# Optimization experiments

Hardware: AMD Instinct MI355X
Metric: run time of the kernel (lower is better)

The kernel has to match this reference:

```python
import jax, jax.numpy as jnp
import numpy as np

D_MODEL = 1024
NUM_HEADS = 16
HEAD_DIM = D_MODEL // NUM_HEADS
ROPE_BASE = 10000.0


def _rope_cos_sin(seq_len, head_dim, dtype):
    # inv_freq over half the head dim (standard 1D RoPE)
    inv_freq = 1.0 / (ROPE_BASE ** (jnp.arange(0, head_dim, 2, dtype=jnp.float32) / head_dim))
    ang = jnp.arange(seq_len, dtype=jnp.float32)[:, None] * inv_freq[None, :]  # [S, hd/2]
    cos = jnp.concatenate([jnp.cos(ang), jnp.cos(ang)], axis=-1).astype(dtype)  # [S, hd]
    sin = jnp.concatenate([jnp.sin(ang), jnp.sin(ang)], axis=-1).astype(dtype)
    return cos, sin


def _rotate_half(t):
    t1, t2 = jnp.split(t, 2, axis=-1)
    return jnp.concatenate([-t2, t1], axis=-1)


def _apply_rope(t, cos, sin):
    # t: [B, H, S, hd]; cos/sin: [S, hd]
    return t * cos[None, None, :, :] + _rotate_half(t) * sin[None, None, :, :]


def setup_inputs() -> dict:
    key = jax.random.key(0)
    k1, k2, k3 = jax.random.split(key, 3)
    B, S = 2, 2048
    x = jax.random.normal(k1, (B, S, D_MODEL), dtype=jnp.float32)
    w_qkv = jax.random.normal(k2, (D_MODEL, 3 * D_MODEL), dtype=jnp.float32) * (D_MODEL ** -0.5)
    w_proj = jax.random.normal(k3, (D_MODEL, D_MODEL), dtype=jnp.float32) * (D_MODEL ** -0.5)
    b_proj = jnp.zeros((D_MODEL,), dtype=jnp.float32)
    return {"x": x, "w_qkv": w_qkv, "w_proj": w_proj, "b_proj": b_proj, "causal": 1}


def reference(x, w_qkv, w_proj, b_proj, causal):
    B, S, D = x.shape
    scale = HEAD_DIM ** -0.5
    qkv = x @ w_qkv  # [B, S, 3D]
    q, k, v = jnp.split(qkv, 3, axis=-1)

    def to_heads(t):
        return t.reshape(B, S, NUM_HEADS, HEAD_DIM).transpose(0, 2, 1, 3)  # [B,H,S,hd]

    q, k, v = to_heads(q), to_heads(k), to_heads(v)

    cos, sin = _rope_cos_sin(S, HEAD_DIM, x.dtype)
    q = _apply_rope(q, cos, sin)
    k = _apply_rope(k, cos, sin)

    attn = jnp.einsum('bhqd,bhkd->bhqk', q, k) * scale  # [B,H,S,S]
    if causal:
        causal_mask = jnp.triu(jnp.ones((S, S), dtype=bool), k=1)
        attn = jnp.where(causal_mask[None, None, :, :], jnp.float32(-jnp.inf).astype(attn.dtype), attn)
    attn = jax.nn.softmax(attn, axis=-1)
    out = jnp.einsum('bhqk,bhkd->bhqd', attn, v)  # [B,H,S,hd]
    out = out.transpose(0, 2, 1, 3).reshape(B, S, D)
    return out @ w_proj + b_proj
```

## Files before the change

### kernel.cpp

```cpp
#include <hip/hip_runtime.h>
#include <stdint.h>
#include <math.h>

#define B_   2
#define S_   2048
#define D_   1024
#define H_   16
#define HD_  64
#define M_   (B_*S_)
#define N3_  (3*D_)

typedef __bf16 bf16;
typedef __bf16 bf16x2 __attribute__((ext_vector_type(2)));
typedef __bf16 bf16x4v __attribute__((ext_vector_type(4)));
typedef __bf16 bf16x8 __attribute__((ext_vector_type(8)));
typedef float  f32x4 __attribute__((ext_vector_type(4)));
typedef float  f32x16 __attribute__((ext_vector_type(16)));

__device__ __forceinline__ void gload_lds16(const void* g, void* l) {
  __builtin_amdgcn_global_load_lds(
      (__attribute__((address_space(1))) const unsigned int*)g,
      (__attribute__((address_space(3))) unsigned int*)l, 16, 0, 0);
}

__device__ __forceinline__ float fast_exp2(float x) {
  return __builtin_amdgcn_exp2f(x);
}

__global__ __launch_bounds__(256) void prep_kernel(const float* __restrict__ x, bf16* __restrict__ xb,
                                                   const float* __restrict__ w_qkv, bf16* __restrict__ wqkvT,
                                                   const float* __restrict__ w_proj, bf16* __restrict__ wprojT,
                                                   float* __restrict__ cosT, float* __restrict__ sinT) {
  __shared__ float tile[32][33];
  int blk = blockIdx.x, tid = threadIdx.x;
  if (blk < 1024) {
#pragma unroll
    for (int it = 0; it < 4; it++) {
      int i = (blk * 4 + it) * 256 + tid;
      float4 v = ((const float4*)x)[i];
      bf16x4v o;
      o[0] = (bf16)v.x; o[1] = (bf16)v.y; o[2] = (bf16)v.z; o[3] = (bf16)v.w;
      *(bf16x4v*)(xb + (size_t)i * 4) = o;
    }
  } else if (blk < 5120) {
    const float* in; bf16* out; int R, C, tb;
    if (blk < 4096) { in = w_qkv;  out = wqkvT;  R = 1024; C = 3072; tb = blk - 1024; }
    else            { in = w_proj; out = wprojT; R = 1024; C = 1024; tb = blk - 4096; }
    int nbx = C >> 5;
    int bx = tb % nbx, by = tb / nbx;
    int c0 = bx * 32, r0 = by * 32;
    int tx = tid & 31, ty = tid >> 5;
#pragma unroll
    for (int j = 0; j < 4; j++)
      tile[ty + j * 8][tx] = in[(size_t)(r0 + ty + j * 8) * C + c0 + tx];
    __syncthreads();
#pragma unroll
    for (int j = 0; j < 4; j++)
      out[(size_t)(c0 + ty + j * 8) * R + r0 + tx] = (bf16)tile[tx][ty + j * 8];
  } else {
    int i = (blk - 5120) * 256 + tid;
    int s = i >> 5, d = i & 31;
    float inv = powf(10000.0f, -(float)d * (1.0f / 32.0f));
    float a = (float)s * inv;
    float sv, cv;
    sincosf(a, &sv, &cv);
    cosT[i] = cv; sinT[i] = sv;
  }
}

__global__ __launch_bounds__(512, 2) void gemm_qkv(const bf16* __restrict__ A,
                                                   const bf16* __restrict__ Bt,
                                                   bf16* __restrict__ Cb,
                                                   const float* __restrict__ cosT,
                                                   const float* __restrict__ sinT,
                                                   bf16* __restrict__ vt) {
  __shared__ __align__(16) unsigned char lds[131072];
  const int K = 1024;
  int tid = threadIdx.x, lane = tid & 63, w = tid >> 6;
  int wm = w >> 2, wn = w & 3;
  int bid = blockIdx.y * gridDim.x + blockIdx.x;
  int sw = (bid & 7) * 24 + (bid >> 3);
  int bx = sw % 12, by = sw / 12;
  int m0 = by * 256, n0 = bx * 256;
  int rl = lane & 15, kg = lane >> 4;

  int l3 = lane >> 3;
  int cS = ((lane & 7) ^ l3) * 16;
  const char* sA = (const char*)A  + ((size_t)(m0 + w * 32 + l3) * K) * 2 + cS;
  const char* sB = (const char*)Bt + ((size_t)(n0 + w * 32 + l3) * K) * 2 + cS;
  char* dA = (char*)lds + w * 4096 + lane * 16;
  char* dB = dA + 32768;

#define STG(kt, s)                                                                   \
  do {                                                                               \
    const int _j = (s) & 3;                                                          \
    const int _bo = ((kt) & 1) << 16;                                                \
    if ((s) < 4) gload_lds16(sA + (size_t)_j * 16384 + (size_t)(kt) * 128,           \
                             dA + _bo + _j * 1024);                                  \
    else         gload_lds16(sB + (size_t)_j * 16384 + (size_t)(kt) * 128,           \
                             dB + _bo + _j * 1024);                                  \
  } while (0)

  int chunkv[2];
  chunkv[0] = ((0 + kg) ^ (rl & 7)) * 16;
  chunkv[1] = ((4 + kg) ^ (rl & 7)) * 16;
  int base_a = (wm * 128 + rl) * 128;
  int base_b = 32768 + (wn * 64 + rl) * 128;

#define RDA(Lb, ar, ks) (*(const bf16x8*)((Lb) + base_a + (ar) * 2048 + chunkv[ks]))
#define RDB(Lb, br, ks) (*(const bf16x8*)((Lb) + base_b + (br) * 2048 + chunkv[ks]))
#define BARR() asm volatile("s_barrier" ::: "memory")
#define VM2()  asm volatile("s_waitcnt vmcnt(2)" ::: "memory")

  f32x4 acc[8][4] = {};
  bf16x8 a[4][2], b[4][2];

#pragma unroll
  for (int s = 0; s < 8; s++) { STG(0, s); STG(1, s); }
  asm volatile("s_waitcnt vmcnt(0)" ::: "memory");
  BARR();

  for (int i = 0; i < 8; i++) {
    int t0 = 2 * i, t1 = t0 + 1;
    const char* L0 = (const char*)lds;
    const char* L1 = (const char*)lds + 65536;

    VM2();
#pragma unroll
    for (int ar = 0; ar < 4; ar++) { a[ar][0] = RDA(L0, ar, 0); a[ar][1] = RDA(L0, ar, 1); }
#pragma unroll
    for (int br = 0; br < 2; br++) { b[br][0] = RDB(L0, br, 0); b[br][1] = RDB(L0, br, 1); }
    if (i) { STG(t1, 2); STG(t1, 3); }
    BARR();
    __builtin_amdgcn_s_setprio(1);
#pragma unroll
    for (int ar = 0; ar < 4; ar++)
#pragma unroll
      for (int br = 0; br < 2; br++) {
        acc[ar][br] = __builtin_amdgcn_mfma_f32_16x16x32_bf16(a[ar][0], b[br][0], acc[ar][br], 0, 0, 0);
        acc[ar][br] = __builtin_amdgcn_mfma_f32_16x16x32_bf16(a[ar][1], b[br][1], acc[ar][br], 0, 0, 0);
      }
    __builtin_amdgcn_s_setprio(0);
    BARR();

#pragma unroll
    for (int br = 2; br < 4; br++) { b[br][0] = RDB(L0, br, 0); b[br][1] = RDB(L0, br, 1); }
    if (i) { STG(t1, 4); STG(t1, 5); }
    BARR();
    __builtin_amdgcn_s_setprio(1);
#pragma unroll
    for (int ar = 0; ar < 4; ar++)
#pragma unroll
      for (int br = 2; br < 4; br++) {
        acc[ar][br] = __builtin_amdgcn_mfma_f32_16x16x32_bf16(a[ar][0], b[br][0], acc[ar][br], 0, 0, 0);
        acc[ar][br] = __builtin_amdgcn_mfma_f32_16x16x32_bf16(a[ar][1], b[br][1], acc[ar][br], 0, 0, 0);
      }
    __builtin_amdgcn_s_setprio(0);
    BARR();

#pragma unroll
    for (int ar = 0; ar < 4; ar++) { a[ar][0] = RDA(L0, ar + 4, 0); a[ar][1] = RDA(L0, ar + 4, 1); }
    if (i) { STG(t1, 6); STG(t1, 7); }
    BARR();
    __builtin_amdgcn_s_setprio(1);
#pragma unroll
    for (int ar = 0; ar < 4; ar++)
#pragma unroll
      for (int br = 0; br < 2; br++) {
        acc[ar + 4][br] = __builtin_amdgcn_mfma_f32_16x16x32_bf16(a[ar][0], b[br][0], acc[ar + 4][br], 0, 0, 0);
        acc[ar + 4][br] = __builtin_amdgcn_mfma_f32_16x16x32_bf16(a[ar][1], b[br][1], acc[ar + 4][br], 0, 0, 0);
      }
    __builtin_amdgcn_s_setprio(0);
    BARR();

    if (t0 + 2 < 16) { STG(t0 + 2, 0); STG(t0 + 2, 1); }
    BARR();
    __builtin_amdgcn_s_setprio(1);
#pragma unroll
    for (int ar = 0; ar < 4; ar++)
#pragma unroll
      for (int br = 2; br < 4; br++) {
        acc[ar + 4][br] = __builtin_amdgcn_mfma_f32_16x16x32_bf16(a[ar][0], b[br][0], acc[ar + 4][br], 0, 0, 0);
        acc[ar + 4][br] = __builtin_amdgcn_mfma_f32_16x16x32_bf16(a[ar][1], b[br][1], acc[ar + 4][br], 0, 0, 0);
      }
    __builtin_amdgcn_s_setprio(0);
    BARR();

    VM2();
#pragma unroll
    for (int ar = 0; ar < 4; ar++) { a[ar][0] = RDA(L1, ar, 0); a[ar][1] = RDA(L1, ar, 1); }
#pragma unroll
    for (int br = 0; br < 2; br++) { b[br][0] = RDB(L1, br, 0); b[br][1] = RDB(L1, br, 1); }
    if (t0 + 2 < 16) { STG(t0 + 2, 2); STG(t0 + 2, 3); }
    BARR();
    __builtin_amdgcn_s_setprio(1);
#pragma unroll
    for (int ar = 0; ar < 4; ar++)
#pragma unroll
      for (int br = 0; br < 2; br++) {
        acc[ar][br] = __builtin_amdgcn_mfma_f32_16x16x32_bf16(a[ar][0], b[br][0], acc[ar][br], 0, 0, 0);
        acc[ar][br] = __builtin_amdgcn_mfma_f32_16x16x32_bf16(a[ar][1], b[br][1], acc[ar][br], 0, 0, 0);
      }
    __builtin_amdgcn_s_setprio(0);
    BARR();

#pragma unroll
    for (int br = 2; br < 4; br++) { b[br][0] = RDB(L1, br, 0); b[br][1] = RDB(L1, br, 1); }
    if (t0 + 2 < 16) { STG(t0 + 2, 4); STG(t0 + 2, 5); }
    BARR();
    __builtin_amdgcn_s_setprio(1);
#pragma unroll
    for (int ar = 0; ar < 4; ar++)
#pragma unroll
      for (int br = 2; br < 4; br++) {
        acc[ar][br] = __builtin_amdgcn_mfma_f32_16x16x32_bf16(a[ar][0], b[br][0], acc[ar][br], 0, 0, 0);
        acc[ar][br] = __builtin_amdgcn_mfma_f32_16x16x32_bf16(a[ar][1], b[br][1], acc[ar][br], 0, 0, 0);
      }
    __builtin_amdgcn_s_setprio(0);
    BARR();

#pragma unroll
    for (int ar = 0; ar < 4; ar++) { a[ar][0] = RDA(L1, ar + 4, 0); a[ar][1] = RDA(L1, ar + 4, 1); }
    if (t0 + 2 < 16) { STG(t0 + 2, 6); STG(t0 + 2, 7); }
    BARR();
    __builtin_amdgcn_s_setprio(1);
#pragma unroll
    for (int ar = 0; ar < 4; ar++)
#pragma unroll
      for (int br = 0; br < 2; br++) {
        acc[ar + 4][br] = __builtin_amdgcn_mfma_f32_16x16x32_bf16(a[ar][0], b[br][0], acc[ar + 4][br], 0, 0, 0);
        acc[ar + 4][br] = __builtin_amdgcn_mfma_f32_16x16x32_bf16(a[ar][1], b[br][1], acc[ar + 4][br], 0, 0, 0);
      }
    __builtin_amdgcn_s_setprio(0);
    BARR();

    if (t1 + 2 < 16) { STG(t1 + 2, 0); STG(t1 + 2, 1); }
    BARR();
    __builtin_amdgcn_s_setprio(1);
#pragma unroll
    for (int ar = 0; ar < 4; ar++)
#pragma unroll
      for (int br = 2; br < 4; br++) {
        acc[ar + 4][br] = __builtin_amdgcn_mfma_f32_16x16x32_bf16(a[ar][0], b[br][0], acc[ar + 4][br], 0, 0, 0);
        acc[ar + 4][br] = __builtin_amdgcn_mfma_f32_16x16x32_bf16(a[ar][1], b[br][1], acc[ar + 4][br], 0, 0, 0);
      }
    __builtin_amdgcn_s_setprio(0);
    BARR();
  }

  int rq = kg * 4;
  if (n0 < 2048) {
#pragma unroll
    for (int ar = 0; ar < 8; ar++)
#pragma unroll
      for (int r = 0; r < 4; r++) {
        int row = m0 + wm * 128 + ar * 16 + rq + r;
        int srw = row & 2047;
#pragma unroll
        for (int br = 0; br < 2; br++) {
          int d2 = br * 16 + rl;
          float c = cosT[srw * 32 + d2], sn = sinT[srw * 32 + d2];
          float x1 = acc[ar][br][r], x2 = acc[ar][br + 2][r];
          size_t o = (size_t)row * 3072 + n0 + wn * 64 + d2;
          Cb[o]      = (bf16)(x1 * c - x2 * sn);
          Cb[o + 32] = (bf16)(x2 * c + x1 * sn);
        }
      }
  } else {
    int posbase = ((rq & 4) << 1) | ((rq & 8) >> 1);
#pragma unroll
    for (int ar = 0; ar < 8; ar++) {
      int row0 = m0 + wm * 128 + ar * 16;
      int bb = row0 >> 11;
      int sbase = (row0 & 2047) + posbase;
#pragma unroll
      for (int br = 0; br < 4; br++) {
        int col = n0 + wn * 64 + br * 16 + rl - 2048;
        bf16x4v pv;
        pv[0] = (bf16)acc[ar][br][0]; pv[1] = (bf16)acc[ar][br][1];
        pv[2] = (bf16)acc[ar][br][2]; pv[3] = (bf16)acc[ar][br][3];
        *(bf16x4v*)(vt + ((size_t)(bb * 1024 + col)) * 2048 + sbase) = pv;
      }
    }
  }
#undef STG
#undef RDA
#undef RDB
#undef BARR
#undef VM2
}

__global__ __launch_bounds__(256) void gemm_proj(const bf16* __restrict__ A,
                                                 const bf16* __restrict__ Bt,
                                                 float* __restrict__ Cf,
                                                 const float* __restrict__ bias) {
  __shared__ bf16 As[64 * 32];
  __shared__ bf16 Bs[128 * 32];
  const int K = 1024, N = 1024;
  int tid = threadIdx.x;
  int lane = tid & 63, w = tid >> 6;
  int bid = blockIdx.y * gridDim.x + blockIdx.x;
  int sw = (bid & 7) * 64 + (bid >> 3);
  int bx = sw & 7, by = sw >> 3;
  int m0 = by * 64, n0 = bx * 128;
  int m_off = (w >> 1) * 32, n_off = (w & 1) * 64;
  f32x4 acc[2][4] = {};

  const char* Ab = (const char*)A;
  const char* Bb = (const char*)Bt;
  int arow = tid >> 2, achk = (tid & 3) * 16;

  for (int k0 = 0; k0 < K; k0 += 32) {
    gload_lds16(Ab + ((size_t)(m0 + arow) * K + k0) * 2 + achk, (char*)As + tid * 16);
    gload_lds16(Bb + ((size_t)(n0 + arow) * K + k0) * 2 + achk, (char*)Bs + tid * 16);
    gload_lds16(Bb + ((size_t)(n0 + 64 + arow) * K + k0) * 2 + achk, (char*)Bs + 4096 + tid * 16);
    __syncthreads();
    int rl = lane & 15;
    int kgb = (lane >> 4) * 16;
    bf16x8 a[2], b[4];
    for (int i = 0; i < 2; i++)
      a[i] = *(const bf16x8*)((const char*)As + (m_off + i * 16 + rl) * 64 + kgb);
    for (int j = 0; j < 4; j++)
      b[j] = *(const bf16x8*)((const char*)Bs + (n_off + j * 16 + rl) * 64 + kgb);
    for (int i = 0; i < 2; i++)
      for (int j = 0; j < 4; j++)
        acc[i][j] = __builtin_amdgcn_mfma_f32_16x16x32_bf16(a[i], b[j], acc[i][j], 0, 0, 0);
    __syncthreads();
  }

  int rq = (lane >> 4) * 4, cl = lane & 15;
  for (int i = 0; i < 2; i++)
    for (int j = 0; j < 4; j++) {
      int col = n0 + n_off + j * 16 + cl;
      float bv = bias[col];
      for (int r = 0; r < 4; r++) {
        int row = m0 + m_off + i * 16 + rq + r;
        Cf[(size_t)row * N + col] = acc[i][j][r] + bv;
      }
    }
}

__global__ __launch_bounds__(512, 4) void attn_kernel(const bf16* __restrict__ qkv,
                                                      const bf16* __restrict__ vt,
                                                      bf16* __restrict__ O) {
  __shared__ __align__(16) unsigned char Ks[2][16384];
  __shared__ __align__(16) unsigned char Vs[2][16384];
  int tid = threadIdx.x, lane = tid & 63, w = tid >> 6;
  int qw = w & 3, p = w >> 2;
  int bid = blockIdx.x;
  int xcd = bid & 7, slot = bid >> 3;
  int bh = xcd * 4 + (slot & 3);
  int u = slot >> 2;
  int qt = 15 - u;
  int b = bh >> 4, h = bh & 15;
  int q0w = qt * 128 + qw * 32;
  int l31 = lane & 31, hi = lane >> 5;
  const char* qb = (const char*)qkv;
  const char* vb = (const char*)vt;

  int kr0 = tid >> 3, kcs = (tid & 7) ^ (kr0 & 7);
  int vr0 = tid >> 4, vcs = (tid & 15) ^ (vr0 & 7);

#define STAGE(buf, kvbase)                                                                              \
  do {                                                                                                  \
    gload_lds16(qb + (((size_t)(b * 2048 + (kvbase) + kr0) * 3072) + 1024 + h * 64) * 2 + kcs * 16,     \
                (char*)Ks[buf] + tid * 16);                                                             \
    gload_lds16(qb + (((size_t)(b * 2048 + (kvbase) + kr0 + 64) * 3072) + 1024 + h * 64) * 2 + kcs * 16,\
                (char*)Ks[buf] + (tid + 512) * 16);                                                     \
    gload_lds16(vb + (((size_t)(bh * 64 + vr0) * 2048) + (kvbase)) * 2 + vcs * 16,                      \
                (char*)Vs[buf] + tid * 16);                                                             \
    gload_lds16(vb + (((size_t)(bh * 64 + vr0 + 32) * 2048) + (kvbase)) * 2 + vcs * 16,                 \
                (char*)Vs[buf] + (tid + 512) * 16);                                                     \
  } while (0)

  bf16x8 aq[4];
#pragma unroll
  for (int s = 0; s < 4; s++) {
    size_t row = (size_t)(b * 2048 + q0w + l31);
    bf16x8 v = *(const bf16x8*)(qb + (row * 3072 + h * 64 + s * 16 + hi * 8) * 2);
#pragma unroll
    for (int e = 0; e < 8; e++) v[e] = (bf16)((float)v[e] * 0.18033688f);
    aq[s] = v;
  }

  f32x16 o0 = {}, o1 = {};
  float mrun = -3e38f, lrun = 0.f;
  int npair = qt + 1;

  STAGE(0, 0);
  asm volatile("s_waitcnt vmcnt(0)" ::: "memory");
  __builtin_amdgcn_s_barrier();

  for (int i = 0; i < npair; i++) {
    int cur = i & 1;
    if (i + 1 < npair) STAGE(cur ^ 1, (i + 1) * 128);

    int kvw = i * 128 + p * 64;
    if (kvw <= q0w + 31) {
      bool diag = (kvw + 63 > q0w);

      f32x16 scr[2];
#pragma unroll
      for (int kf = 0; kf < 2; kf++)
#pragma unroll
        for (int r = 0; r < 16; r++) scr[kf][r] = 0.f;
      __builtin_amdgcn_s_setprio(1);
#pragma unroll
      for (int s = 0; s < 4; s++) {
#pragma unroll
        for (int kf = 0; kf < 2; kf++) {
          int row = p * 64 + kf * 32 + l31;
          int ch = (hi + 2 * s) ^ (row & 7);
          bf16x8 ak = *(const bf16x8*)(Ks[cur] + row * 128 + ch * 16);
          scr[kf] = __builtin_amdgcn_mfma_f32_32x32x16_bf16(ak, aq[s], scr[kf], 0, 0, 0);
        }
      }
      __builtin_amdgcn_s_setprio(0);

      int qg = q0w + l31;
      if (diag) {
#pragma unroll
        for (int kf = 0; kf < 2; kf++)
#pragma unroll
          for (int r = 0; r < 16; r++) {
            int k = kvw + kf * 32 + (r & 3) + 8 * (r >> 2) + 4 * hi;
            if (k > qg) scr[kf][r] = -3e38f;
          }
      }

      float mx = -3e38f;
#pragma unroll
      for (int kf = 0; kf < 2; kf++)
#pragma unroll
        for (int r = 0; r < 16; r++) mx = fmaxf(mx, scr[kf][r]);
      mx = fmaxf(mx, __shfl_xor(mx, 32));

      if (!__all(mx - mrun <= 11.5f)) {
        float mnew = fmaxf(mrun, mx);
        float corr = exp2f(mrun - mnew);
        mrun = mnew;
        lrun *= corr;
#pragma unroll
        for (int r = 0; r < 16; r++) {
          float cr = __shfl(corr, (r & 3) + 8 * (r >> 2) + 4 * hi);
          o0[r] *= cr; o1[r] *= cr;
        }
      }

      float rs = 0.f;
      unsigned D[2][8];
#pragma unroll
      for (int kf = 0; kf < 2; kf++)
#pragma unroll
        for (int j = 0; j < 8; j++) {
          float p0 = fast_exp2(scr[kf][2 * j] - mrun);
          float p1 = fast_exp2(scr[kf][2 * j + 1] - mrun);
          rs += p0 + p1;
          bf16x2 tp; tp[0] = (bf16)p0; tp[1] = (bf16)p1;
          D[kf][j] = __builtin_bit_cast(unsigned, tp);
        }
      rs += __shfl_xor(rs, 32);
      lrun += rs;

#pragma unroll
      for (int kf = 0; kf < 2; kf++) {
#pragma unroll
        for (int sg = 0; sg < 2; sg++) {
          union { unsigned u4[4]; bf16x8 v; } ap;
          ap.u4[0] = D[kf][4 * sg + 0];
          ap.u4[1] = D[kf][4 * sg + 1];
          ap.u4[2] = D[kf][4 * sg + 2];
          ap.u4[3] = D[kf][4 * sg + 3];
          __builtin_amdgcn_s_setprio(1);
#pragma unroll
          for (int nf = 0; nf < 2; nf++) {
            int row = nf * 32 + l31;
            int ch = ((p * 8) + (hi + 2 * sg + 4 * kf)) ^ (row & 7);
            bf16x8 bv = *(const bf16x8*)(Vs[cur] + row * 256 + ch * 16);
            if (nf == 0) o0 = __builtin_amdgcn_mfma_f32_32x32x16_bf16(ap.v, bv, o0, 0, 0, 0);
            else         o1 = __builtin_amdgcn_mfma_f32_32x32x16_bf16(ap.v, bv, o1, 0, 0, 0);
          }
          __builtin_amdgcn_s_setprio(0);
        }
      }
    }

    asm volatile("s_waitcnt vmcnt(0)" ::: "memory");
    __builtin_amdgcn_s_barrier();
  }

  float* mlb = (float*)Ks;
  if (hi == 0) {
    mlb[((qw * 2 + p) * 2 + 0) * 32 + l31] = mrun;
    mlb[((qw * 2 + p) * 2 + 1) * 32 + l31] = lrun;
  }
  __syncthreads();
  float m_o = mlb[((qw * 2 + (1 - p)) * 2 + 0) * 32 + l31];
  float l_o = mlb[((qw * 2 + (1 - p)) * 2 + 1) * 32 + l31];
  float Mm = fmaxf(mrun, m_o);
  float cs = exp2f(mrun - Mm);
  float L  = lrun * cs + l_o * exp2f(m_o - Mm);
  float* obuf = (float*)Vs;
  if (p == 1) {
#pragma unroll
    for (int r = 0; r < 16; r++) {
      int crow = (r & 3) + 8 * (r >> 2) + 4 * hi;
      float c = __shfl(cs, crow);
      obuf[qw * 2048 + r * 64 + lane]        = o0[r] * c;
      obuf[qw * 2048 + (r + 16) * 64 + lane] = o1[r] * c;
    }
  }
  __syncthreads();
  if (p == 0) {
    float linv = 1.0f / L;
#pragma unroll
    for (int r = 0; r < 16; r++) {
      int crow = (r & 3) + 8 * (r >> 2) + 4 * hi;
      float c  = __shfl(cs, crow);
      float li = __shfl(linv, crow);
      size_t row = (size_t)(b * 2048 + q0w + crow);
      float v0 = (o0[r] * c + obuf[qw * 2048 + r * 64 + lane]) * li;
      float v1 = (o1[r] * c + obuf[qw * 2048 + (r + 16) * 64 + lane]) * li;
      O[row * 1024 + h * 64 + l31]      = (bf16)v0;
      O[row * 1024 + h * 64 + 32 + l31] = (bf16)v1;
    }
  }
#undef STAGE
}

extern "C" void kernel_launch(void* const* d_in, const int* in_sizes, int n_in,
                              void* d_out, int out_size, void* d_ws, size_t ws_size,
                              hipStream_t stream) {
  const float* x      = (const float*)d_in[0];
  const float* w_qkv  = (const float*)d_in[1];
  const float* w_proj = (const float*)d_in[2];
  const float* b_proj = (const float*)d_in[3];

  char* ws = (char*)d_ws;
  size_t off = 0;
  bf16* xb     = (bf16*)(ws + off); off += (size_t)M_ * D_ * 2;
  bf16* wqkvT  = (bf16*)(ws + off); off += (size_t)N3_ * D_ * 2;
  bf16* wprojT = (bf16*)(ws + off); off += (size_t)D_ * D_ * 2;
  bf16* qkvb   = (bf16*)(ws + off); off += (size_t)M_ * N3_ * 2;
  bf16* ob     = (bf16*)(ws + off); off += (size_t)M_ * D_ * 2;
  bf16* vtb    = (bf16*)(ws + off); off += (size_t)M_ * D_ * 2;
  float* cosT  = (float*)(ws + off); off += (size_t)S_ * 32 * 4;
  float* sinT  = (float*)(ws + off); off += (size_t)S_ * 32 * 4;

  prep_kernel<<<5376, 256, 0, stream>>>(x, xb, w_qkv, wqkvT, w_proj, wprojT, cosT, sinT);
  gemm_qkv<<<dim3(12, 16), 512, 0, stream>>>(xb, wqkvT, qkvb, cosT, sinT, vtb);
  attn_kernel<<<512, 512, 0, stream>>>(qkvb, vtb, ob);
  gemm_proj<<<dim3(8, 64), 256, 0, stream>>>(ob, wprojT, (float*)d_out, b_proj);
}
```

Before: 103.8 us.

## Double K-tile depth in projection GEMM with XOR-swizzled LDS layout

The output projection GEMM now loads a K depth of 64 per iteration instead of 32, which halves the number of barrier pairs over the K loop. The 16-byte chunks in LDS are XOR-swizzled by row to avoid bank conflicts on the wider 128-byte rows, and the MFMA block is wrapped in s_setprio to favour math issue. The cost is more LDS per block and more registers for the doubled fragments, which may lower occupancy.

Result: no change. 102.1 us (-1.6%).

```diff
diff --git a/kernel.cpp b/kernel.cpp
--- a/kernel.cpp
+++ b/kernel.cpp
@@ -294,8 +294,8 @@
                                                  const bf16* __restrict__ Bt,
                                                  float* __restrict__ Cf,
                                                  const float* __restrict__ bias) {
-  __shared__ bf16 As[64 * 32];
-  __shared__ bf16 Bs[128 * 32];
+  __shared__ __align__(16) unsigned char As[8192];
+  __shared__ __align__(16) unsigned char Bs[16384];
   const int K = 1024, N = 1024;
   int tid = threadIdx.x;
   int lane = tid & 63, w = tid >> 6;
@@ -304,34 +304,58 @@
   int bx = sw & 7, by = sw >> 3;
   int m0 = by * 64, n0 = bx * 128;
   int m_off = (w >> 1) * 32, n_off = (w & 1) * 64;
+  int rl = lane & 15, kg = lane >> 4;
   f32x4 acc[2][4] = {};
 
   const char* Ab = (const char*)A;
   const char* Bb = (const char*)Bt;
-  int arow = tid >> 2, achk = (tid & 3) * 16;
-
-  for (int k0 = 0; k0 < K; k0 += 32) {
-    gload_lds16(Ab + ((size_t)(m0 + arow) * K + k0) * 2 + achk, (char*)As + tid * 16);
-    gload_lds16(Bb + ((size_t)(n0 + arow) * K + k0) * 2 + achk, (char*)Bs + tid * 16);
-    gload_lds16(Bb + ((size_t)(n0 + 64 + arow) * K + k0) * 2 + achk, (char*)Bs + 4096 + tid * 16);
+  int r8 = tid >> 3;
+  int cSw = ((tid & 7) ^ (r8 & 7)) * 16;
+
+  int ch0 = ((0 + kg) ^ (rl & 7)) * 16;
+  int ch1 = ((4 + kg) ^ (rl & 7)) * 16;
+
+  for (int k0 = 0; k0 < K; k0 += 64) {
+#pragma unroll
+    for (int s = 0; s < 2; s++) {
+      int row = s * 32 + r8;
+      gload_lds16(Ab + ((size_t)(m0 + row) * K + k0) * 2 + cSw, (char*)As + s * 4096 + tid * 16);
+    }
+#pragma unroll
+    for (int s = 0; s < 4; s++) {
+      int row = s * 32 + r8;
+      gload_lds16(Bb + ((size_t)(n0 + row) * K + k0) * 2 + cSw, (char*)Bs + s * 4096 + tid * 16);
+    }
     __syncthreads();
-    int rl = lane & 15;
-    int kgb = (lane >> 4) * 16;
-    bf16x8 a[2], b[4];
+    bf16x8 a[2][2], b[4][2];
+#pragma unroll
+    for (int i = 0; i < 2; i++) {
+      int row = m_off + i * 16 + rl;
+      a[i][0] = *(const bf16x8*)((const char*)As + row * 128 + ch0);
+      a[i][1] = *(const bf16x8*)((const char*)As + row * 128 + ch1);
+    }
+#pragma unroll
+    for (int j = 0; j < 4; j++) {
+      int row = n_off + j * 16 + rl;
+      b[j][0] = *(const bf16x8*)((const char*)Bs + row * 128 + ch0);
+      b[j][1] = *(const bf16x8*)((const char*)Bs + row * 128 + ch1);
+    }
+    __builtin_amdgcn_s_setprio(1);
+#pragma unroll
     for (int i = 0; i < 2; i++)
-      a[i] = *(const bf16x8*)((const char*)As + (m_off + i * 16 + rl) * 64 + kgb);
-    for (int j = 0; j < 4; j++)
-      b[j] = *(const bf16x8*)((const char*)Bs + (n_off + j * 16 + rl) * 64 + kgb);
-    for (int i = 0; i < 2; i++)
-      for (int j = 0; j < 4; j++)
-        acc[i][j] = __builtin_amdgcn_mfma_f32_16x16x32_bf16(a[i], b[j], acc[i][j], 0, 0, 0);
+#pragma unroll
+      for (int j = 0; j < 4; j++) {
+        acc[i][j] = __builtin_amdgcn_mfma_f32_16x16x32_bf16(a[i][0], b[j][0], acc[i][j], 0, 0, 0);
+        acc[i][j] = __builtin_amdgcn_mfma_f32_16x16x32_bf16(a[i][1], b[j][1], acc[i][j], 0, 0, 0);
+      }
+    __builtin_amdgcn_s_setprio(0);
     __syncthreads();
   }
 
-  int rq = (lane >> 4) * 4, cl = lane & 15;
+  int rq = kg * 4;
   for (int i = 0; i < 2; i++)
     for (int j = 0; j < 4; j++) {
-      int col = n0 + n_off + j * 16 + cl;
+      int col = n0 + n_off + j * 16 + rl;
       float bv = bias[col];
       for (int r = 0; r < 4; r++) {
         int row = m0 + m_off + i * 16 + rq + r;
```
